# Performance work log

Measured on AMD Instinct MI355X. Metric: run time of the kernel, lower is better.

## Reference

```python
import jax, jax.numpy as jnp
import numpy as np
from jax import lax

WINDOW_SIZE = 11
SIGMA = 1.5
C1 = 0.01 ** 2
C2 = 0.03 ** 2


def _gaussian_window(window_size: int, sigma: float) -> jnp.ndarray:
    coords = jnp.arange(window_size, dtype=jnp.float32) - window_size // 2
    g = jnp.exp(-0.5 * (coords / sigma) ** 2)
    g = g / g.sum()
    return g[:, None] * g[None, :]  # (ws, ws)


def _dwconv(x, win2d):
    # x: (B, C, H, W); win2d: (ws, ws). Depthwise conv, same padding.
    c = x.shape[1]
    ws = win2d.shape[0]
    pad = ws // 2
    k = jnp.broadcast_to(win2d[None, None], (c, 1, ws, ws))  # (O=C, I/g=1, ws, ws)
    return lax.conv_general_dilated(
        x, k, window_strides=(1, 1), padding=[(pad, pad), (pad, pad)],
        dimension_numbers=('NCHW', 'OIHW', 'NCHW'), feature_group_count=c)


def setup_inputs() -> dict:
    key = jax.random.key(0)
    k1, k2 = jax.random.split(key)
    shape = (32, 3, 512, 512)
    img1 = jax.random.uniform(k1, shape, dtype=jnp.float32)
    img2 = jax.random.uniform(k2, shape, dtype=jnp.float32)
    return {"img1": img1, "img2": img2}


def reference(img1, img2):
    win = _gaussian_window(WINDOW_SIZE, SIGMA).astype(img1.dtype)
    mu1 = _dwconv(img1, win)
    mu2 = _dwconv(img2, win)
    mu1_sq = mu1 * mu1
    mu2_sq = mu2 * mu2
    mu12 = mu1 * mu2
    sigma1_sq = _dwconv(img1 * img1, win) - mu1_sq
    sigma2_sq = _dwconv(img2 * img2, win) - mu2_sq
    sigma12 = _dwconv(img1 * img2, win) - mu12
    numerator = (2.0 * mu12 + C1) * (2.0 * sigma12 + C2)
    denominator = (mu1_sq + mu2_sq + C1) * (sigma1_sq + sigma2_sq + C2)
    ssim_map = numerator / denominator
    return 1.0 - ssim_map.mean()
```

## Files before the change

kernel.cpp:

```cpp
#include <hip/hip_runtime.h>
#include <hip/hip_bf16.h>

#define IMG   512
#define TW    64
#define TH    32
#define WS    11
#define NP    96
#define NSLOT 256
#define PR    21
#define PLANE (PR*64)

static __device__ __forceinline__ ushort f2bf(float x) {
    __hip_bfloat16 h = __float2bfloat16(x);
    return __builtin_bit_cast(ushort, h);
}
static __device__ __forceinline__ uint pkbf(float ev, float od) {
    return (uint)f2bf(ev) | ((uint)f2bf(od) << 16);
}
static __device__ __forceinline__ float bfval(ushort u) {
    return __builtin_bit_cast(float, (uint)u << 16);
}

__global__ __launch_bounds__(256, 4) void ssim_main(const float* __restrict__ img1,
                                                    const float* __restrict__ img2,
                                                    double* __restrict__ acc) {
    constexpr float W[WS] = {
        0.00102837990674f, 0.00759883148699f, 0.03600079242909f,
        0.10936069869137f, 0.21300538108707f, 0.26601190869814f,
        0.21300538108707f, 0.10936069869137f, 0.03600079242909f,
        0.00759883148699f, 0.00102837990674f };

    __shared__ uint HP[5 * PLANE];

    const int tid = threadIdx.x;
    const int bx = blockIdx.x;
    const int by = blockIdx.y;
    const float* p1 = img1 + (size_t)blockIdx.z * (IMG * IMG);
    const float* p2 = img2 + (size_t)blockIdx.z * (IMG * IMG);

    ushort us[12];
    #pragma unroll
    for (int t = 0; t < WS; ++t) us[t] = f2bf(W[t]);
    us[11] = 0;
    float alpha = 0.f;
    #pragma unroll
    for (int t = 0; t < WS; ++t) alpha += bfval(us[t]);
    uint pe[6], po[6];
    #pragma unroll
    for (int j = 0; j < 6; ++j) {
        pe[j] = (uint)us[2*j] | ((uint)us[2*j+1] << 16);
        po[j] = (j ? (uint)us[2*j-1] : 0u) | ((uint)us[2*j] << 16);
    }

    for (int u = tid; u < PR * 16; u += 256) {
        const int pr = u >> 4;
        const int cg = u & 15;

        float A[5][2][4];
        #pragma unroll
        for (int s = 0; s < 5; ++s)
            #pragma unroll
            for (int rw = 0; rw < 2; ++rw)
                #pragma unroll
                for (int o = 0; o < 4; ++o) A[s][rw][o] = 0.f;

        #pragma unroll
        for (int rw = 0; rw < 2; ++rw) {
            const int gy = by * TH + 2 * pr + rw - 5;
            const bool rowOK = (unsigned)gy < IMG;
            const float* r1 = p1 + (size_t)gy * IMG;
            const float* r2 = p2 + (size_t)gy * IMG;
            #pragma unroll
            for (int j = 0; j < 5; ++j) {
                const int gx = bx * TW + cg * 4 - 8 + 4 * j;
                float4 X = make_float4(0.f,0.f,0.f,0.f), Y = X;
                if (rowOK && (unsigned)gx < IMG) {
                    X = *(const float4*)(r1 + gx);
                    Y = *(const float4*)(r2 + gx);
                }
                const float e1[4] = {X.x,X.y,X.z,X.w};
                const float e2[4] = {Y.x,Y.y,Y.z,Y.w};
                #pragma unroll
                for (int e = 0; e < 4; ++e) {
                    const int i = 4*j + e;
                    if (i < 3 || i > 16) continue;
                    const float x1 = e1[e], x2 = e2[e];
                    const float q11 = x1*x1, q22 = x2*x2, q12 = x1*x2;
                    #pragma unroll
                    for (int o = 0; o < 4; ++o) {
                        const int t = i - 3 - o;
                        if (t >= 0 && t < WS) {
                            A[0][rw][o] += W[t]*x1;  A[1][rw][o] += W[t]*x2;
                            A[2][rw][o] += W[t]*q11; A[3][rw][o] += W[t]*q22;
                            A[4][rw][o] += W[t]*q12;
                        }
                    }
                }
            }
        }

        #pragma unroll
        for (int s = 0; s < 5; ++s) {
            const uint4 pv = make_uint4(pkbf(A[s][0][0], A[s][1][0]),
                                        pkbf(A[s][0][1], A[s][1][1]),
                                        pkbf(A[s][0][2], A[s][1][2]),
                                        pkbf(A[s][0][3], A[s][1][3]));
            *(uint4*)&HP[(s * PR + pr) * 64 + cg * 4] = pv;
        }
    }
    __syncthreads();

    const int q0 = tid >> 4;
    const int cg = tid & 15;

    float m[5][2][4];
    #pragma unroll
    for (int s = 0; s < 5; ++s)
        #pragma unroll
        for (int pth = 0; pth < 2; ++pth)
            #pragma unroll
            for (int c = 0; c < 4; ++c) m[s][pth][c] = 0.f;

    #pragma unroll
    for (int s = 0; s < 5; ++s) {
        #pragma unroll
        for (int j = 0; j <= 5; ++j) {
            const uint4 v = *(const uint4*)&HP[(s * PR + q0 + j) * 64 + cg * 4];
            const uint vv[4] = {v.x, v.y, v.z, v.w};
            #pragma unroll
            for (int c = 0; c < 4; ++c) {
                asm("v_dot2_f32_bf16 %0, %1, %2, %0"
                    : "+v"(m[s][0][c]) : "v"(vv[c]), "v"(pe[j]));
                asm("v_dot2_f32_bf16 %0, %1, %2, %0"
                    : "+v"(m[s][1][c]) : "v"(vv[c]), "v"(po[j]));
            }
        }
    }

    const float invA = 1.0f / alpha;
    const float C1 = 0.01f*0.01f, C2 = 0.03f*0.03f;
    float lsum = 0.f;
    #pragma unroll
    for (int pth = 0; pth < 2; ++pth) {
        #pragma unroll
        for (int c = 0; c < 4; ++c) {
            const float mu1 = m[0][pth][c] * invA, mu2 = m[1][pth][c] * invA;
            const float m11 = m[2][pth][c] * invA, m22 = m[3][pth][c] * invA;
            const float m12 = m[4][pth][c] * invA;
            const float mu1s = mu1*mu1, mu2s = mu2*mu2, mu12 = mu1*mu2;
            const float s11 = m11 - mu1s;
            const float s22 = m22 - mu2s;
            const float s12 = m12 - mu12;
            const float num = (2.f*mu12 + C1) * (2.f*s12 + C2);
            const float den = (mu1s + mu2s + C1) * (s11 + s22 + C2);
            lsum += num * __builtin_amdgcn_rcpf(den);
        }
    }

    #pragma unroll
    for (int d = 32; d >= 1; d >>= 1)
        lsum += __shfl_down(lsum, d, 64);
    __shared__ float wsum[4];
    if ((tid & 63) == 0) wsum[tid >> 6] = lsum;
    __syncthreads();
    if (tid == 0) {
        const float t = wsum[0] + wsum[1] + wsum[2] + wsum[3];
        const int bid = (blockIdx.z * gridDim.y + blockIdx.y) * gridDim.x + blockIdx.x;
        atomicAdd(&acc[bid & (NSLOT - 1)], (double)t);
    }
}

__global__ void ssim_final(const double* __restrict__ acc, float* __restrict__ out) {
    const int l = threadIdx.x;
    double s = acc[l] + acc[l + 64] + acc[l + 128] + acc[l + 192];
    #pragma unroll
    for (int d = 32; d >= 1; d >>= 1)
        s += __shfl_down(s, d, 64);
    if (l == 0)
        out[0] = 1.0f - (float)(s / (double)((size_t)NP * IMG * IMG));
}

extern "C" void kernel_launch(void* const* d_in, const int* in_sizes, int n_in,
                              void* d_out, int out_size, void* d_ws, size_t ws_size,
                              hipStream_t stream) {
    const float* img1 = (const float*)d_in[0];
    const float* img2 = (const float*)d_in[1];
    float* out = (float*)d_out;
    double* acc = (double*)d_ws;

    hipMemsetAsync(d_ws, 0, NSLOT * sizeof(double), stream);

    dim3 grid(IMG / TW, IMG / TH, NP);
    ssim_main<<<grid, dim3(256), 0, stream>>>(img1, img2, acc);
    ssim_final<<<1, dim3(64), 0, stream>>>(acc, out);
}
```

Baseline: 112.9 us.

## Use taller 32x64 tiles and fp16 packing for the vertical pass

Changes the tile shape from 64x32 to 32x64 so the vertical halo is amortized over more rows, reducing packed row-pairs per output. Switches the intermediate horizontal-pass storage from bf16 to fp16 using packed round-toward-zero conversion and fp16 dot2 instructions, improving precision. Narrower rows may reduce global load coalescing efficiency.

```diff
diff --git a/kernel.cpp b/kernel.cpp
--- a/kernel.cpp
+++ b/kernel.cpp
@@ -1,24 +1,26 @@
 #include <hip/hip_runtime.h>
-#include <hip/hip_bf16.h>
+#include <hip/hip_fp16.h>
 
 #define IMG   512
-#define TW    64
-#define TH    32
+#define TW    32
+#define TH    64
 #define WS    11
 #define NP    96
 #define NSLOT 256
-#define PR    21
-#define PLANE (PR*64)
+#define PR2   37
+#define RSTR  32
+#define PLANE (PR2*RSTR)
 
-static __device__ __forceinline__ ushort f2bf(float x) {
-    __hip_bfloat16 h = __float2bfloat16(x);
-    return __builtin_bit_cast(ushort, h);
+typedef __attribute__((ext_vector_type(2))) _Float16 half2v;
+
+static __device__ __forceinline__ uint pkh(float ev, float od) {
+    return __builtin_bit_cast(uint, __builtin_amdgcn_cvt_pkrtz(ev, od));
 }
-static __device__ __forceinline__ uint pkbf(float ev, float od) {
-    return (uint)f2bf(ev) | ((uint)f2bf(od) << 16);
+static __device__ __forceinline__ ushort f2h(float x) {
+    return __builtin_bit_cast(ushort, (_Float16)x);
 }
-static __device__ __forceinline__ float bfval(ushort u) {
-    return __builtin_bit_cast(float, (uint)u << 16);
+static __device__ __forceinline__ float h2f(ushort u) {
+    return (float)__builtin_bit_cast(_Float16, u);
 }
 
 __global__ __launch_bounds__(256, 4) void ssim_main(const float* __restrict__ img1,
@@ -40,11 +42,11 @@
 
     ushort us[12];
     #pragma unroll
-    for (int t = 0; t < WS; ++t) us[t] = f2bf(W[t]);
+    for (int t = 0; t < WS; ++t) us[t] = f2h(W[t]);
     us[11] = 0;
     float alpha = 0.f;
     #pragma unroll
-    for (int t = 0; t < WS; ++t) alpha += bfval(us[t]);
+    for (int t = 0; t < WS; ++t) alpha += h2f(us[t]);
     uint pe[6], po[6];
     #pragma unroll
     for (int j = 0; j < 6; ++j) {
@@ -52,9 +54,9 @@
         po[j] = (j ? (uint)us[2*j-1] : 0u) | ((uint)us[2*j] << 16);
     }
 
-    for (int u = tid; u < PR * 16; u += 256) {
-        const int pr = u >> 4;
-        const int cg = u & 15;
+    for (int u = tid; u < PR2 * 8; u += 256) {
+        const int pr = u >> 3;
+        const int cg = u & 7;
 
         float A[5][2][4];
         #pragma unroll
@@ -101,17 +103,17 @@
 
         #pragma unroll
         for (int s = 0; s < 5; ++s) {
-            const uint4 pv = make_uint4(pkbf(A[s][0][0], A[s][1][0]),
-                                        pkbf(A[s][0][1], A[s][1][1]),
-                                        pkbf(A[s][0][2], A[s][1][2]),
-                                        pkbf(A[s][0][3], A[s][1][3]));
-            *(uint4*)&HP[(s * PR + pr) * 64 + cg * 4] = pv;
+            const uint4 pv = make_uint4(pkh(A[s][0][0], A[s][1][0]),
+                                        pkh(A[s][0][1], A[s][1][1]),
+                                        pkh(A[s][0][2], A[s][1][2]),
+                                        pkh(A[s][0][3], A[s][1][3]));
+            *(uint4*)&HP[(s * PR2 + pr) * RSTR + cg * 4] = pv;
         }
     }
     __syncthreads();
 
-    const int q0 = tid >> 4;
-    const int cg = tid & 15;
+    const int q0 = tid >> 3;
+    const int cg = tid & 7;
 
     float m[5][2][4];
     #pragma unroll
@@ -125,13 +127,13 @@
     for (int s = 0; s < 5; ++s) {
         #pragma unroll
         for (int j = 0; j <= 5; ++j) {
-            const uint4 v = *(const uint4*)&HP[(s * PR + q0 + j) * 64 + cg * 4];
+            const uint4 v = *(const uint4*)&HP[(s * PR2 + q0 + j) * RSTR + cg * 4];
             const uint vv[4] = {v.x, v.y, v.z, v.w};
             #pragma unroll
             for (int c = 0; c < 4; ++c) {
-                asm("v_dot2_f32_bf16 %0, %1, %2, %0"
+                asm("v_dot2_f32_f16 %0, %1, %2, %0"
                     : "+v"(m[s][0][c]) : "v"(vv[c]), "v"(pe[j]));
-                asm("v_dot2_f32_bf16 %0, %1, %2, %0"
+                asm("v_dot2_f32_f16 %0, %1, %2, %0"
                     : "+v"(m[s][1][c]) : "v"(vv[c]), "v"(po[j]));
             }
         }
```

Result: faster. 106.7 us (-5.6%).
